# Kernel optimization log

Measured on AMD Instinct MI355X. Metric: run time of the kernel, lower is better.

Reference implementation:

```python
import jax, jax.numpy as jnp
import numpy as np

T, E, H, I = 4096, 8, 2048, 4096  # tokens, experts, hidden, intermediate


def setup_inputs() -> dict:
    key = jax.random.key(0)
    k1, k2, k3, k4 = jax.random.split(key, 4)
    return {
        "hidden_states": jax.random.normal(k1, (T, H), dtype=jnp.float32),
        "router_logits": jax.random.normal(k2, (T, E), dtype=jnp.float32),
        # W13: [E, hidden, 2*inter] (post-transpose layout; cols [0:I]=W1 gate, [I:2I]=W3 up)
        "W13": jax.random.normal(k3, (E, H, 2 * I), dtype=jnp.float32) * 0.02,
        # W2: [E, inter, hidden]
        "W2": jax.random.normal(k4, (E, I, H), dtype=jnp.float32) * 0.02,
        "top_k": 2,
    }


def reference(hidden_states, router_logits, W13, W2, top_k):
    # topk_softmax routing (use_grouped_topk=False, renormalize=True)
    probs = jax.nn.softmax(router_logits, axis=-1)              # [T, E]
    w, idx = jax.lax.top_k(probs, top_k)                        # [T, k]
    w = w / jnp.sum(w, axis=-1, keepdims=True)                  # renormalize
    # dense combine weights per (token, expert): equivalent to scatter->grouped gemm->gather
    tok = jnp.arange(hidden_states.shape[0])[:, None]
    comb = jnp.zeros_like(probs).at[tok, idx].add(w)            # [T, E]

    def expert_step(acc, xs):
        W13_e, W2_e, cw = xs                                    # [H,2I], [I,H], [T]
        h = hidden_states @ W13_e                               # [T, 2I]
        half = h.shape[-1] // 2
        a = jax.nn.silu(h[:, :half]) * h[:, half:]              # fused SiLU-mul
        o = a @ W2_e                                            # [T, H]
        return acc + cw[:, None] * o, None

    out, _ = jax.lax.scan(expert_step, jnp.zeros_like(hidden_states), (W13, W2, comb.T))
    return out
```

## Files before the change

### kernel.cpp

```cpp
#include <hip/hip_runtime.h>
#include <hip/hip_bf16.h>

#define T_TOK 4096
#define NEXP 8
#define HID 2048
#define INTER 4096
#define NPAIR (2 * T_TOK)

typedef unsigned int u32;
typedef unsigned short u16;
typedef short s16x8 __attribute__((ext_vector_type(8)));
typedef float f32x4 __attribute__((ext_vector_type(4)));

#define LSTRIDE 40
#define BK 32
#define ASZ (128 * LSTRIDE)

__device__ __forceinline__ u16 f2bf(float a) {
  u32 u = __builtin_bit_cast(u32, a);
  return (u16)((u + 0x7fffu + ((u >> 16) & 1u)) >> 16);
}
__device__ __forceinline__ u32 pk2(float a, float b) {
  return (u32)f2bf(a) | ((u32)f2bf(b) << 16);
}

#define BARRIER() asm volatile("s_waitcnt lgkmcnt(0)\ns_barrier" ::: "memory")

__global__ void zero_cnt_k(int* cnt) {
  if (threadIdx.x < NEXP) cnt[threadIdx.x] = 0;
}

__global__ void zero_out_k(float* out) {
  size_t i = ((size_t)blockIdx.x * blockDim.x + threadIdx.x) * 4;
  *(float4*)(out + i) = make_float4(0.f, 0.f, 0.f, 0.f);
}

__global__ void route_k(const float* __restrict__ logits, int* cnt,
                        int* eids, int* ranks, float* wts) {
  int t = blockIdx.x * blockDim.x + threadIdx.x;
  if (t >= T_TOK) return;
  float l[NEXP];
#pragma unroll
  for (int i = 0; i < NEXP; ++i) l[i] = logits[t * NEXP + i];
  int i0 = 0; float m0 = l[0];
#pragma unroll
  for (int i = 1; i < NEXP; ++i) if (l[i] > m0) { m0 = l[i]; i0 = i; }
  int i1 = -1; float m1 = -3.4e38f;
#pragma unroll
  for (int i = 0; i < NEXP; ++i) if (i != i0 && l[i] > m1) { m1 = l[i]; i1 = i; }
  float p1 = __expf(m1 - m0);
  float w0 = 1.f / (1.f + p1);
  float w1 = p1 * w0;
  int r0 = atomicAdd(&cnt[i0], 1);
  int r1 = atomicAdd(&cnt[i1], 1);
  eids[2 * t] = i0;  eids[2 * t + 1] = i1;
  ranks[2 * t] = r0; ranks[2 * t + 1] = r1;
  wts[2 * t] = w0;   wts[2 * t + 1] = w1;
}

__global__ void scan_k(const int* cnt, int* off) {
  if (threadIdx.x == 0 && blockIdx.x == 0) {
    int a = 0;
    for (int e = 0; e < NEXP; ++e) { off[e] = a; a += cnt[e]; }
  }
}

__global__ void place_k(const int* __restrict__ off, const int* __restrict__ eids,
                        const int* __restrict__ ranks, const float* __restrict__ wts,
                        int* __restrict__ tok, float* __restrict__ wgt) {
  int t = blockIdx.x * blockDim.x + threadIdx.x;
  if (t >= T_TOK) return;
#pragma unroll
  for (int s = 0; s < 2; ++s) {
    int e = eids[2 * t + s];
    int p = off[e] + ranks[2 * t + s];
    tok[p] = t;
    wgt[p] = wts[2 * t + s];
  }
}

__global__ __launch_bounds__(512, 4) void gemm1_k(
    const float* __restrict__ X, const float* __restrict__ W13,
    const int* __restrict__ cnt, const int* __restrict__ off,
    const int* __restrict__ tok, u16* __restrict__ Abuf) {
  const int id = ((blockIdx.x & 7) << 11) | ((int)blockIdx.x >> 3);
  const int rt = id & 31;
  const int ct = (id >> 5) & 63;
  const int e  = id >> 11;
  const int n_e = cnt[e];
  if (rt * 128 >= n_e) return;
  const int off_e = off[e];

  __shared__ __align__(16) u16 Ls[2][2][ASZ];

  const int tid = threadIdx.x;
  const int wid = tid >> 6;
  const int lane = tid & 63;
  const int q = lane >> 4;
  const int l15 = lane & 15;
  const int wr = wid >> 1;
  const int wc = wid & 1;

  const int arow = tid >> 2, aseg = tid & 3;
  int ridx = rt * 128 + arow;
  if (ridx >= n_e) ridx = n_e - 1;
  const float* aptr = X + (size_t)tok[off_e + ridx] * HID + aseg * 8;
  const int adoff = arow * LSTRIDE + aseg * 8;

  const int c = tid & 127, ks = tid >> 7;
  const size_t colb = (c < 64) ? (size_t)(ct * 64 + c)
                               : (size_t)(INTER + ct * 64 + (c - 64));
  const float* bptr = W13 + (size_t)e * ((size_t)HID * (2 * INTER))
                    + (size_t)(ks * 8) * (2 * INTER) + colb;
  const int bdoff = c * LSTRIDE + ks * 8;

  const int afoff = (32 * wr + l15) * LSTRIDE + q * 8;
  const int bfoff = (32 * wc + l15) * LSTRIDE + q * 8;

  f32x4 acc[2][4];
#pragma unroll
  for (int i = 0; i < 2; ++i)
#pragma unroll
    for (int j = 0; j < 4; ++j) acc[i][j] = (f32x4){0.f, 0.f, 0.f, 0.f};

  float a_f[8], b_f[8];

#define G1_LOAD(k0_)                                                         \
  { const float* ap_ = aptr + (k0_);                                         \
    float4 t0_ = *(const float4*)ap_;                                        \
    float4 t1_ = *(const float4*)(ap_ + 4);                                  \
    a_f[0]=t0_.x; a_f[1]=t0_.y; a_f[2]=t0_.z; a_f[3]=t0_.w;                  \
    a_f[4]=t1_.x; a_f[5]=t1_.y; a_f[6]=t1_.z; a_f[7]=t1_.w;                  \
    const float* bp_ = bptr + (size_t)(k0_) * (2 * INTER);                   \
    b_f[0]=bp_[0*(size_t)(2*INTER)]; b_f[1]=bp_[1*(size_t)(2*INTER)];        \
    b_f[2]=bp_[2*(size_t)(2*INTER)]; b_f[3]=bp_[3*(size_t)(2*INTER)];        \
    b_f[4]=bp_[4*(size_t)(2*INTER)]; b_f[5]=bp_[5*(size_t)(2*INTER)];        \
    b_f[6]=bp_[6*(size_t)(2*INTER)]; b_f[7]=bp_[7*(size_t)(2*INTER)]; }

#define G1_PW(wb_)                                                           \
  { uint4 wa_ = make_uint4(pk2(a_f[0],a_f[1]), pk2(a_f[2],a_f[3]),           \
                           pk2(a_f[4],a_f[5]), pk2(a_f[6],a_f[7]));          \
    uint4 wv_ = make_uint4(pk2(b_f[0],b_f[1]), pk2(b_f[2],b_f[3]),           \
                           pk2(b_f[4],b_f[5]), pk2(b_f[6],b_f[7]));          \
    *(uint4*)&Ls[wb_][0][adoff] = wa_;                                       \
    *(uint4*)&Ls[wb_][1][bdoff] = wv_; }

#define G1_FM(rb_)                                                           \
  { const u16* Ab_ = Ls[rb_][0]; const u16* Bb_ = Ls[rb_][1];                \
    s16x8 af0 = *(const s16x8*)&Ab_[afoff];                                  \
    s16x8 af1 = *(const s16x8*)&Ab_[afoff + 16 * LSTRIDE];                   \
    s16x8 b0 = *(const s16x8*)&Bb_[bfoff];                                   \
    s16x8 b1 = *(const s16x8*)&Bb_[bfoff + 16 * LSTRIDE];                    \
    s16x8 b2 = *(const s16x8*)&Bb_[bfoff + 64 * LSTRIDE];                    \
    s16x8 b3 = *(const s16x8*)&Bb_[bfoff + 80 * LSTRIDE];                    \
    acc[0][0] = __builtin_amdgcn_mfma_f32_16x16x32_bf16(af0, b0, acc[0][0], 0, 0, 0); \
    acc[1][0] = __builtin_amdgcn_mfma_f32_16x16x32_bf16(af1, b0, acc[1][0], 0, 0, 0); \
    acc[0][1] = __builtin_amdgcn_mfma_f32_16x16x32_bf16(af0, b1, acc[0][1], 0, 0, 0); \
    acc[1][1] = __builtin_amdgcn_mfma_f32_16x16x32_bf16(af1, b1, acc[1][1], 0, 0, 0); \
    acc[0][2] = __builtin_amdgcn_mfma_f32_16x16x32_bf16(af0, b2, acc[0][2], 0, 0, 0); \
    acc[1][2] = __builtin_amdgcn_mfma_f32_16x16x32_bf16(af1, b2, acc[1][2], 0, 0, 0); \
    acc[0][3] = __builtin_amdgcn_mfma_f32_16x16x32_bf16(af0, b3, acc[0][3], 0, 0, 0); \
    acc[1][3] = __builtin_amdgcn_mfma_f32_16x16x32_bf16(af1, b3, acc[1][3], 0, 0, 0); }

  const int NT = HID / BK;
  G1_LOAD(0);
  G1_PW(0);
  G1_LOAD(BK);
  BARRIER();
#pragma unroll 2
  for (int t = 0; t < NT; ++t) {
    G1_FM(t & 1);
    if (t + 1 < NT) {
      G1_PW((t + 1) & 1);
      int kn = (t + 2) * BK;
      if (kn > HID - BK) kn = HID - BK;
      G1_LOAD(kn);
      BARRIER();
    }
  }

  const int rb = rt * 128 + 32 * wr + q * 4;
#pragma unroll
  for (int rf = 0; rf < 2; ++rf) {
#pragma unroll
    for (int r = 0; r < 4; ++r) {
      const int grow = rb + 16 * rf + r;
      if (grow < n_e) {
        u16* ad = Abuf + (size_t)(off_e + grow) * INTER + (ct * 64 + 32 * wc + l15);
        float g0 = acc[rf][0][r], u0 = acc[rf][2][r];
        float g1 = acc[rf][1][r], u1 = acc[rf][3][r];
        ad[0]  = f2bf(g0 / (1.f + __expf(-g0)) * u0);
        ad[16] = f2bf(g1 / (1.f + __expf(-g1)) * u1);
      }
    }
  }
#undef G1_LOAD
#undef G1_PW
#undef G1_FM
}

__global__ __launch_bounds__(512, 4) void gemm2_k(
    const u16* __restrict__ Abuf, const float* __restrict__ W2,
    const int* __restrict__ cnt, const int* __restrict__ off,
    const int* __restrict__ tok, const float* __restrict__ wgt,
    float* __restrict__ out) {
  const int id = ((blockIdx.x & 7) << 9) | ((int)blockIdx.x >> 3);
  const int rt = id & 31;
  const int ct = (id >> 5) & 15;
  const int e  = id >> 9;
  const int n_e = cnt[e];
  if (rt * 128 >= n_e) return;
  const int off_e = off[e];

  __shared__ __align__(16) u16 Ls[2][2][ASZ];

  const int tid = threadIdx.x;
  const int wid = tid >> 6;
  const int lane = tid & 63;
  const int q = lane >> 4;
  const int l15 = lane & 15;
  const int wr = wid >> 1;
  const int wc = wid & 1;

  const int arow = tid >> 2, aseg = tid & 3;
  int ridx = rt * 128 + arow;
  if (ridx >= n_e) ridx = n_e - 1;
  const u16* aptr = Abuf + (size_t)(off_e + ridx) * INTER + aseg * 8;
  const int adoff = arow * LSTRIDE + aseg * 8;

  const int c = tid & 127, ks = tid >> 7;
  const float* bptr = W2 + (size_t)e * ((size_t)INTER * HID)
                    + (size_t)(ks * 8) * HID + (ct * 128 + c);
  const int bdoff = c * LSTRIDE + ks * 8;

  const int afoff = (32 * wr + l15) * LSTRIDE + q * 8;
  const int bfoff = (64 * wc + l15) * LSTRIDE + q * 8;

  f32x4 acc[2][4];
#pragma unroll
  for (int i = 0; i < 2; ++i)
#pragma unroll
    for (int j = 0; j < 4; ++j) acc[i][j] = (f32x4){0.f, 0.f, 0.f, 0.f};

  uint4 a_u;
  float b_f[8];

#define G2_LOAD(k0_)                                                         \
  { a_u = *(const uint4*)(aptr + (k0_));                                     \
    const float* bp_ = bptr + (size_t)(k0_) * HID;                           \
    b_f[0]=bp_[0*(size_t)HID]; b_f[1]=bp_[1*(size_t)HID];                    \
    b_f[2]=bp_[2*(size_t)HID]; b_f[3]=bp_[3*(size_t)HID];                    \
    b_f[4]=bp_[4*(size_t)HID]; b_f[5]=bp_[5*(size_t)HID];                    \
    b_f[6]=bp_[6*(size_t)HID]; b_f[7]=bp_[7*(size_t)HID]; }

#define G2_PW(wb_)                                                           \
  { uint4 wv_ = make_uint4(pk2(b_f[0],b_f[1]), pk2(b_f[2],b_f[3]),           \
                           pk2(b_f[4],b_f[5]), pk2(b_f[6],b_f[7]));          \
    *(uint4*)&Ls[wb_][0][adoff] = a_u;                                       \
    *(uint4*)&Ls[wb_][1][bdoff] = wv_; }

#define G2_FM(rb_)                                                           \
  { const u16* Ab_ = Ls[rb_][0]; const u16* Bb_ = Ls[rb_][1];                \
    s16x8 af0 = *(const s16x8*)&Ab_[afoff];                                  \
    s16x8 af1 = *(const s16x8*)&Ab_[afoff + 16 * LSTRIDE];                   \
    s16x8 b0 = *(const s16x8*)&Bb_[bfoff];                                   \
    s16x8 b1 = *(const s16x8*)&Bb_[bfoff + 16 * LSTRIDE];                    \
    s16x8 b2 = *(const s16x8*)&Bb_[bfoff + 32 * LSTRIDE];                    \
    s16x8 b3 = *(const s16x8*)&Bb_[bfoff + 48 * LSTRIDE];                    \
    acc[0][0] = __builtin_amdgcn_mfma_f32_16x16x32_bf16(af0, b0, acc[0][0], 0, 0, 0); \
    acc[1][0] = __builtin_amdgcn_mfma_f32_16x16x32_bf16(af1, b0, acc[1][0], 0, 0, 0); \
    acc[0][1] = __builtin_amdgcn_mfma_f32_16x16x32_bf16(af0, b1, acc[0][1], 0, 0, 0); \
    acc[1][1] = __builtin_amdgcn_mfma_f32_16x16x32_bf16(af1, b1, acc[1][1], 0, 0, 0); \
    acc[0][2] = __builtin_amdgcn_mfma_f32_16x16x32_bf16(af0, b2, acc[0][2], 0, 0, 0); \
    acc[1][2] = __builtin_amdgcn_mfma_f32_16x16x32_bf16(af1, b2, acc[1][2], 0, 0, 0); \
    acc[0][3] = __builtin_amdgcn_mfma_f32_16x16x32_bf16(af0, b3, acc[0][3], 0, 0, 0); \
    acc[1][3] = __builtin_amdgcn_mfma_f32_16x16x32_bf16(af1, b3, acc[1][3], 0, 0, 0); }

  const int NT = INTER / BK;
  G2_LOAD(0);
  G2_PW(0);
  G2_LOAD(BK);
  BARRIER();
#pragma unroll 2
  for (int t = 0; t < NT; ++t) {
    G2_FM(t & 1);
    if (t + 1 < NT) {
      G2_PW((t + 1) & 1);
      int kn = (t + 2) * BK;
      if (kn > INTER - BK) kn = INTER - BK;
      G2_LOAD(kn);
      BARRIER();
    }
  }

  const int rb = rt * 128 + 32 * wr + q * 4;
#pragma unroll
  for (int rf = 0; rf < 2; ++rf) {
#pragma unroll
    for (int r = 0; r < 4; ++r) {
      const int grow = rb + 16 * rf + r;
      if (grow < n_e) {
        const int p = off_e + grow;
        const int tkn = tok[p];
        const float w = wgt[p];
        float* orow = out + (size_t)tkn * HID + (ct * 128 + 64 * wc + l15);
        atomicAdd(orow + 0,  w * acc[rf][0][r]);
        atomicAdd(orow + 16, w * acc[rf][1][r]);
        atomicAdd(orow + 32, w * acc[rf][2][r]);
        atomicAdd(orow + 48, w * acc[rf][3][r]);
      }
    }
  }
#undef G2_LOAD
#undef G2_PW
#undef G2_FM
}

extern "C" void kernel_launch(void* const* d_in, const int* in_sizes, int n_in,
                              void* d_out, int out_size, void* d_ws, size_t ws_size,
                              hipStream_t stream) {
  const float* X      = (const float*)d_in[0];
  const float* logits = (const float*)d_in[1];
  const float* W13    = (const float*)d_in[2];
  const float* W2     = (const float*)d_in[3];
  float* out = (float*)d_out;

  char* ws = (char*)d_ws;
  int* cnt    = (int*)ws;
  int* off    = cnt + NEXP;
  int* eids   = off + NEXP;
  int* ranks  = eids + NPAIR;
  float* wts  = (float*)(ranks + NPAIR);
  int* tokA   = (int*)(wts + NPAIR);
  float* wgtA = (float*)(tokA + NPAIR);
  u16* Abuf   = (u16*)(ws + (1 << 20));

  zero_cnt_k<<<1, 64, 0, stream>>>(cnt);
  zero_out_k<<<(T_TOK * HID) / 1024, 256, 0, stream>>>(out);
  route_k<<<T_TOK / 256, 256, 0, stream>>>(logits, cnt, eids, ranks, wts);
  scan_k<<<1, 64, 0, stream>>>(cnt, off);
  place_k<<<T_TOK / 256, 256, 0, stream>>>(off, eids, ranks, wts, tokA, wgtA);
  gemm1_k<<<NEXP * 64 * 32, 512, 0, stream>>>(X, W13, cnt, off, tokA, Abuf);
  gemm2_k<<<NEXP * 16 * 32, 512, 0, stream>>>(Abuf, W2, cnt, off, tokA, wgtA, out);
}
```

Baseline: 1.754 ms.

## Pre-convert activations and weights to bf16 in k-blocked layout for vector loads

After: 1.655 ms. 1.06x faster.

```diff
diff --git a/kernel.cpp b/kernel.cpp
--- a/kernel.cpp
+++ b/kernel.cpp
@@ -79,8 +79,46 @@
   }
 }
 
+__global__ void convx_k(const float* __restrict__ X, u16* __restrict__ Xbf) {
+  size_t i = (size_t)blockIdx.x * blockDim.x + threadIdx.x;
+  float4 v0 = ((const float4*)X)[i * 2];
+  float4 v1 = ((const float4*)X)[i * 2 + 1];
+  uint4 w = make_uint4(pk2(v0.x, v0.y), pk2(v0.z, v0.w),
+                       pk2(v1.x, v1.y), pk2(v1.z, v1.w));
+  ((uint4*)Xbf)[i] = w;
+}
+
+template <int KDIM, int NDIM>
+__global__ void convw_k(const float* __restrict__ src0, u16* __restrict__ dst0) {
+  const int ntiles = NDIM / 32;
+  const int ktiles = KDIM / 64;
+  const int b = blockIdx.x;
+  const int nt = b % ntiles;
+  const int kt = (b / ntiles) % ktiles;
+  const int e  = b / (ntiles * ktiles);
+  const float* src = src0 + (size_t)e * KDIM * NDIM + (size_t)(kt * 64) * NDIM + nt * 32;
+  uint4* dst = (uint4*)dst0 + (size_t)e * (KDIM / 8) * NDIM;
+
+  __shared__ u32 Lt[32][36];
+
+  const int t = threadIdx.x;
+  const int r = t >> 3;
+  const int c4 = t & 7;
+  float4 v0 = ((const float4*)(src + (size_t)(2 * r) * NDIM))[c4];
+  float4 v1 = ((const float4*)(src + (size_t)(2 * r + 1) * NDIM))[c4];
+  Lt[c4 * 4 + 0][r] = pk2(v0.x, v1.x);
+  Lt[c4 * 4 + 1][r] = pk2(v0.y, v1.y);
+  Lt[c4 * 4 + 2][r] = pk2(v0.z, v1.z);
+  Lt[c4 * 4 + 3][r] = pk2(v0.w, v1.w);
+  __syncthreads();
+  const int n = t >> 3;
+  const int q = t & 7;
+  uint4 w = *(const uint4*)&Lt[n][q * 4];
+  dst[(size_t)(kt * 8 + q) * NDIM + nt * 32 + n] = w;
+}
+
 __global__ __launch_bounds__(512, 4) void gemm1_k(
-    const float* __restrict__ X, const float* __restrict__ W13,
+    const u16* __restrict__ Xbf, const u16* __restrict__ W13T,
     const int* __restrict__ cnt, const int* __restrict__ off,
     const int* __restrict__ tok, u16* __restrict__ Abuf) {
   const int id = ((blockIdx.x & 7) << 11) | ((int)blockIdx.x >> 3);
@@ -104,14 +142,13 @@
   const int arow = tid >> 2, aseg = tid & 3;
   int ridx = rt * 128 + arow;
   if (ridx >= n_e) ridx = n_e - 1;
-  const float* aptr = X + (size_t)tok[off_e + ridx] * HID + aseg * 8;
+  const u16* aptr = Xbf + (size_t)tok[off_e + ridx] * HID + aseg * 8;
   const int adoff = arow * LSTRIDE + aseg * 8;
 
   const int c = tid & 127, ks = tid >> 7;
-  const size_t colb = (c < 64) ? (size_t)(ct * 64 + c)
-                               : (size_t)(INTER + ct * 64 + (c - 64));
-  const float* bptr = W13 + (size_t)e * ((size_t)HID * (2 * INTER))
-                    + (size_t)(ks * 8) * (2 * INTER) + colb;
+  const int colb = (c < 64) ? (ct * 64 + c) : (INTER + ct * 64 + (c - 64));
+  const uint4* bbase = (const uint4*)W13T + (size_t)e * ((size_t)(HID / 8) * (2 * INTER))
+                     + (size_t)ks * (2 * INTER) + colb;
   const int bdoff = c * LSTRIDE + ks * 8;
 
   const int afoff = (32 * wr + l15) * LSTRIDE + q * 8;
@@ -123,27 +160,15 @@
 #pragma unroll
     for (int j = 0; j < 4; ++j) acc[i][j] = (f32x4){0.f, 0.f, 0.f, 0.f};
 
-  float a_f[8], b_f[8];
+  uint4 a_u, b_u;
 
 #define G1_LOAD(k0_)                                                         \
-  { const float* ap_ = aptr + (k0_);                                         \
-    float4 t0_ = *(const float4*)ap_;                                        \
-    float4 t1_ = *(const float4*)(ap_ + 4);                                  \
-    a_f[0]=t0_.x; a_f[1]=t0_.y; a_f[2]=t0_.z; a_f[3]=t0_.w;                  \
-    a_f[4]=t1_.x; a_f[5]=t1_.y; a_f[6]=t1_.z; a_f[7]=t1_.w;                  \
-    const float* bp_ = bptr + (size_t)(k0_) * (2 * INTER);                   \
-    b_f[0]=bp_[0*(size_t)(2*INTER)]; b_f[1]=bp_[1*(size_t)(2*INTER)];        \
-    b_f[2]=bp_[2*(size_t)(2*INTER)]; b_f[3]=bp_[3*(size_t)(2*INTER)];        \
-    b_f[4]=bp_[4*(size_t)(2*INTER)]; b_f[5]=bp_[5*(size_t)(2*INTER)];        \
-    b_f[6]=bp_[6*(size_t)(2*INTER)]; b_f[7]=bp_[7*(size_t)(2*INTER)]; }
+  { a_u = *(const uint4*)(aptr + (k0_));                                     \
+    b_u = bbase[(size_t)((k0_) >> 3) * (2 * INTER)]; }
 
 #define G1_PW(wb_)                                                           \
-  { uint4 wa_ = make_uint4(pk2(a_f[0],a_f[1]), pk2(a_f[2],a_f[3]),           \
-                           pk2(a_f[4],a_f[5]), pk2(a_f[6],a_f[7]));          \
-    uint4 wv_ = make_uint4(pk2(b_f[0],b_f[1]), pk2(b_f[2],b_f[3]),           \
-                           pk2(b_f[4],b_f[5]), pk2(b_f[6],b_f[7]));          \
-    *(uint4*)&Ls[wb_][0][adoff] = wa_;                                       \
-    *(uint4*)&Ls[wb_][1][bdoff] = wv_; }
+  { *(uint4*)&Ls[wb_][0][adoff] = a_u;                                       \
+    *(uint4*)&Ls[wb_][1][bdoff] = b_u; }
 
 #define G1_FM(rb_)                                                           \
   { const u16* Ab_ = Ls[rb_][0]; const u16* Bb_ = Ls[rb_][1];                \
@@ -180,17 +205,20 @@
   }
 
   const int rb = rt * 128 + 32 * wr + q * 4;
+  const int nb = ct * 64 + 32 * wc + l15;
+  const size_t cb0 = (size_t)(nb >> 3) * NPAIR;
+  const int nrem = nb & 7;
 #pragma unroll
   for (int rf = 0; rf < 2; ++rf) {
 #pragma unroll
     for (int r = 0; r < 4; ++r) {
       const int grow = rb + 16 * rf + r;
       if (grow < n_e) {
-        u16* ad = Abuf + (size_t)(off_e + grow) * INTER + (ct * 64 + 32 * wc + l15);
+        const size_t p = (size_t)(off_e + grow);
         float g0 = acc[rf][0][r], u0 = acc[rf][2][r];
         float g1 = acc[rf][1][r], u1 = acc[rf][3][r];
-        ad[0]  = f2bf(g0 / (1.f + __expf(-g0)) * u0);
-        ad[16] = f2bf(g1 / (1.f + __expf(-g1)) * u1);
+        Abuf[(cb0 + p) * 8 + nrem]              = f2bf(g0 / (1.f + __expf(-g0)) * u0);
+        Abuf[(cb0 + 2 * NPAIR + p) * 8 + nrem]  = f2bf(g1 / (1.f + __expf(-g1)) * u1);
       }
     }
   }
@@ -200,7 +228,7 @@
 }
 
 __global__ __launch_bounds__(512, 4) void gemm2_k(
-    const u16* __restrict__ Abuf, const float* __restrict__ W2,
+    const u16* __restrict__ Abuf, const u16* __restrict__ W2T,
     const int* __restrict__ cnt, const int* __restrict__ off,
     const int* __restrict__ tok, const float* __restrict__ wgt,
     float* __restrict__ out) {
@@ -225,12 +253,13 @@
   const int arow = tid >> 2, aseg = tid & 3;
   int ridx = rt * 128 + arow;
   if (ridx >= n_e) ridx = n_e - 1;
-  const u16* aptr = Abuf + (size_t)(off_e + ridx) * INTER + aseg * 8;
+  const size_t p_stage = (size_t)(off_e + ridx);
+  const uint4* abase = (const uint4*)Abuf + (size_t)aseg * NPAIR + p_stage;
   const int adoff = arow * LSTRIDE + aseg * 8;
 
   const int c = tid & 127, ks = tid >> 7;
-  const float* bptr = W2 + (size_t)e * ((size_t)INTER * HID)
-                    + (size_t)(ks * 8) * HID + (ct * 128 + c);
+  const uint4* bbase = (const uint4*)W2T + (size_t)e * ((size_t)(INTER / 8) * HID)
+                     + (size_t)ks * HID + (ct * 128 + c);
   const int bdoff = c * LSTRIDE + ks * 8;
 
   const int afoff = (32 * wr + l15) * LSTRIDE + q * 8;
@@ -242,22 +271,15 @@
 #pragma unroll
     for (int j = 0; j < 4; ++j) acc[i][j] = (f32x4){0.f, 0.f, 0.f, 0.f};
 
-  uint4 a_u;
-  float b_f[8];
+  uint4 a_u, b_u;
 
 #define G2_LOAD(k0_)                                                         \
-  { a_u = *(const uint4*)(aptr + (k0_));                                     \
-    const float* bp_ = bptr + (size_t)(k0_) * HID;                           \
-    b_f[0]=bp_[0*(size_t)HID]; b_f[1]=bp_[1*(size_t)HID];                    \
-    b_f[2]=bp_[2*(size_t)HID]; b_f[3]=bp_[3*(size_t)HID];                    \
-    b_f[4]=bp_[4*(size_t)HID]; b_f[5]=bp_[5*(size_t)HID];                    \
-    b_f[6]=bp_[6*(size_t)HID]; b_f[7]=bp_[7*(size_t)HID]; }
+  { a_u = abase[(size_t)((k0_) >> 3) * NPAIR];                               \
+    b_u = bbase[(size_t)((k0_) >> 3) * HID]; }
 
 #define G2_PW(wb_)                                                           \
-  { uint4 wv_ = make_uint4(pk2(b_f[0],b_f[1]), pk2(b_f[2],b_f[3]),           \
-                           pk2(b_f[4],b_f[5]), pk2(b_f[6],b_f[7]));          \
-    *(uint4*)&Ls[wb_][0][adoff] = a_u;                                       \
-    *(uint4*)&Ls[wb_][1][bdoff] = wv_; }
+  { *(uint4*)&Ls[wb_][0][adoff] = a_u;                                       \
+    *(uint4*)&Ls[wb_][1][bdoff] = b_u; }
 
 #define G2_FM(rb_)                                                           \
   { const u16* Ab_ = Ls[rb_][0]; const u16* Bb_ = Ls[rb_][1];                \
@@ -300,9 +322,9 @@
     for (int r = 0; r < 4; ++r) {
       const int grow = rb + 16 * rf + r;
       if (grow < n_e) {
-        const int p = off_e + grow;
-        const int tkn = tok[p];
-        const float w = wgt[p];
+        const int pp = off_e + grow;
+        const int tkn = tok[pp];
+        const float w = wgt[pp];
         float* orow = out + (size_t)tkn * HID + (ct * 128 + 64 * wc + l15);
         atomicAdd(orow + 0,  w * acc[rf][0][r]);
         atomicAdd(orow + 16, w * acc[rf][1][r]);
@@ -333,13 +355,19 @@
   float* wts  = (float*)(ranks + NPAIR);
   int* tokA   = (int*)(wts + NPAIR);
   float* wgtA = (float*)(tokA + NPAIR);
-  u16* Abuf   = (u16*)(ws + (1 << 20));
+  u16* Xbf  = (u16*)(ws + ((size_t)1 << 20));
+  u16* Abuf = (u16*)(ws + ((size_t)24 << 20));
+  u16* W13T = (u16*)(ws + ((size_t)96 << 20));
+  u16* W2T  = W13T;
 
   zero_cnt_k<<<1, 64, 0, stream>>>(cnt);
   zero_out_k<<<(T_TOK * HID) / 1024, 256, 0, stream>>>(out);
   route_k<<<T_TOK / 256, 256, 0, stream>>>(logits, cnt, eids, ranks, wts);
   scan_k<<<1, 64, 0, stream>>>(cnt, off);
   place_k<<<T_TOK / 256, 256, 0, stream>>>(off, eids, ranks, wts, tokA, wgtA);
-  gemm1_k<<<NEXP * 64 * 32, 512, 0, stream>>>(X, W13, cnt, off, tokA, Abuf);
-  gemm2_k<<<NEXP * 16 * 32, 512, 0, stream>>>(Abuf, W2, cnt, off, tokA, wgtA, out);
-}
+  convx_k<<<(T_TOK * HID / 8) / 256, 256, 0, stream>>>(X, Xbf);
+  convw_k<HID, 2 * INTER><<<NEXP * (HID / 64) * (2 * INTER / 32), 256, 0, stream>>>(W13, W13T);
+  gemm1_k<<<NEXP * 64 * 32, 512, 0, stream>>>(Xbf, W13T, cnt, off, tokA, Abuf);
+  convw_k<INTER, HID><<<NEXP * (INTER / 64) * (HID / 32), 256, 0, stream>>>(W2, W2T);
+  gemm2_k<<<NEXP * 16 * 32, 512, 0, stream>>>(Abuf, W2T, cnt, off, tokA, wgtA, out);
+}
```
